# Optimization experiments

Measured on AMD Instinct MI355X. Metric: run time of the kernel, lower is better.

The kernel has to match this reference:

```python
import jax, jax.numpy as jnp
import numpy as np

B, N, XD = 4, 8192, 256   # batch, seq len, input/kv feature dim
F, H = 512, 8             # features, heads
D = F // H                # per-head dim = 64
EPS = 1e-6                # flax LayerNorm default epsilon


def _layer_norm(t, scale, bias):
    mu = jnp.mean(t, axis=-1, keepdims=True)
    var = jnp.mean(jnp.square(t - mu), axis=-1, keepdims=True)
    return (t - mu) * jax.lax.rsqrt(var + EPS) * scale + bias


def setup_inputs() -> dict:
    key = jax.random.key(0)
    ks = jax.random.split(key, 5)
    return {
        "x": jax.random.normal(ks[0], (B, N, XD), jnp.float32),
        "kv": jax.random.normal(ks[1], (B, N, XD), jnp.float32),
        # linen.initializers.normal(1/x_dim) / normal(1/h_dim)
        "Q": jax.random.normal(ks[2], (XD, F), jnp.float32) * (1.0 / XD),
        "K": jax.random.normal(ks[3], (XD, F), jnp.float32) * (1.0 / XD),
        "V": jax.random.normal(ks[4], (XD, F), jnp.float32) * (1.0 / XD),
        "log_scale": jnp.zeros((F,), jnp.float32),
        "ln_q_scale": jnp.ones((D,), jnp.float32),
        "ln_q_bias": jnp.zeros((D,), jnp.float32),
        "ln_k_scale": jnp.ones((D,), jnp.float32),
        "ln_k_bias": jnp.zeros((D,), jnp.float32),
        "ln_v_scale": jnp.ones((D,), jnp.float32),
        "ln_v_bias": jnp.zeros((D,), jnp.float32),
    }


def reference(x, kv, Q, K, V, log_scale,
              ln_q_scale, ln_q_bias, ln_k_scale, ln_k_bias, ln_v_scale, ln_v_bias):
    # QKV projections (value scaled by exp(log_scale) per feature)
    query = x @ Q                                    # [B, N, F]
    key = kv @ K                                     # [B, N, F]
    value = jnp.exp(log_scale) * (kv @ V)            # [B, N, F]
    # reshape exactly as the source module does
    q = query.reshape(B, H, -1, D)                   # [B, H, N, D]
    k = key.reshape(B, H, -1, D)
    v = value.reshape(B, H, -1, D)
    # per-head LayerNorm over the head dim (layer_norm=True)
    q = _layer_norm(q, ln_q_scale, ln_q_bias)
    k = _layer_norm(k, ln_k_scale, ln_k_bias)
    v = _layer_norm(v, ln_v_scale, ln_v_bias)
    # galerkin linear attention: Q @ (K^T V) / seq_len, no softmax, no NxN scores
    seq_len = k.shape[-2]
    ctx = jnp.einsum('bhnd,bhne->bhde', k, v)        # [B, H, D, D]
    out = jnp.einsum('bhnd,bhde->bhne', q, ctx) / seq_len
    return out.reshape(B, N, F)
```

## Files before the change

### kernel.cpp

```cpp
#include <hip/hip_runtime.h>
#include <stdint.h>

using f32x4  = __attribute__((ext_vector_type(4))) float;
using short8 = __attribute__((ext_vector_type(8))) short;

#define MFMA(a, b, c) __builtin_amdgcn_mfma_f32_16x16x32_bf16((a), (b), (c), 0, 0, 0)

#define GLOBAL_AS __attribute__((address_space(1)))
#define LDS_AS    __attribute__((address_space(3)))

#define XDIM 256
#define FDIM 512
#define EPS  1e-6f

#define QT_OFF    0u
#define KT_OFF    262144u
#define VT_OFF    524288u
#define CTXT_OFF  786432u
#define PART_OFF  1048576u

static __device__ __forceinline__ unsigned short f2bf(float f) {
  unsigned u = __float_as_uint(f);
  unsigned r = u + 0x7FFFu + ((u >> 16) & 1u);
  return (unsigned short)(r >> 16);
}

static __device__ __forceinline__ void async_copy16(const void* g, void* l) {
  __builtin_amdgcn_global_load_lds((GLOBAL_AS const void*)g, (LDS_AS void*)l, 16, 0, 0);
}

static __device__ __forceinline__ void stage_wpanel(const unsigned short* wt_panel, int ks,
                                                    int w, int lane, char* Blds) {
  const int cs = ((lane & 7) ^ ((lane >> 3) & 7)) << 4;
  const char* gbase = (const char*)wt_panel + (size_t)ks * 128 + cs;
#pragma unroll
  for (int i = 0; i < 8; ++i) {
    const int frow = w * 64 + i * 8 + (lane >> 3);
    async_copy16(gbase + (size_t)frow * 512, Blds + (size_t)(w * 64 + i * 8) * 128);
  }
}

static __device__ __forceinline__ void stage_a(const float* a_rows, int ks, int tid, char* Alds) {
  const int r = tid >> 2, cq = tid & 3;
  const float* s = a_rows + (size_t)r * XDIM + ks * 64 + cq * 16;
  float4 f0 = *(const float4*)(s);
  float4 f1 = *(const float4*)(s + 4);
  float4 f2 = *(const float4*)(s + 8);
  float4 f3 = *(const float4*)(s + 12);
  short8 v0, v1;
  v0[0] = (short)f2bf(f0.x); v0[1] = (short)f2bf(f0.y);
  v0[2] = (short)f2bf(f0.z); v0[3] = (short)f2bf(f0.w);
  v0[4] = (short)f2bf(f1.x); v0[5] = (short)f2bf(f1.y);
  v0[6] = (short)f2bf(f1.z); v0[7] = (short)f2bf(f1.w);
  v1[0] = (short)f2bf(f2.x); v1[1] = (short)f2bf(f2.y);
  v1[2] = (short)f2bf(f2.z); v1[3] = (short)f2bf(f2.w);
  v1[4] = (short)f2bf(f3.x); v1[5] = (short)f2bf(f3.y);
  v1[6] = (short)f2bf(f3.z); v1[7] = (short)f2bf(f3.w);
  *(short8*)(Alds + r * 144 + cq * 32)      = v0;
  *(short8*)(Alds + r * 144 + cq * 32 + 16) = v1;
}

static __device__ __forceinline__ void gemm_step(f32x4 acc[4][4], const char* Alds,
                                                 const char* Blds, int w, int lane) {
  const int lr = lane & 15, lk = lane >> 4;
#pragma unroll
  for (int s = 0; s < 2; ++s) {
    short8 a[4], b[4];
#pragma unroll
    for (int mt = 0; mt < 4; ++mt)
      a[mt] = *(const short8*)(Alds + (mt * 16 + lr) * 144 + s * 64 + lk * 16);
#pragma unroll
    for (int nt = 0; nt < 4; ++nt) {
      const int nf = w * 64 + nt * 16 + lr;
      b[nt] = *(const short8*)(Blds + (size_t)nf * 128 + ((s * 64 + lk * 16) ^ ((nf & 7) << 4)));
    }
#pragma unroll
    for (int mt = 0; mt < 4; ++mt)
#pragma unroll
      for (int nt = 0; nt < 4; ++nt)
        acc[mt][nt] = MFMA(a[mt], b[nt], acc[mt][nt]);
  }
}

static __device__ __forceinline__ void chunk_layernorm(f32x4 acc[4][4], const float* sc,
                                                       const float* bs, int lane) {
  const int lr = lane & 15;
  float scl[4], bia[4];
#pragma unroll
  for (int nt = 0; nt < 4; ++nt) { scl[nt] = sc[nt * 16 + lr]; bia[nt] = bs[nt * 16 + lr]; }
#pragma unroll
  for (int mt = 0; mt < 4; ++mt) {
#pragma unroll
    for (int j = 0; j < 4; ++j) {
      float a0 = acc[mt][0][j], a1 = acc[mt][1][j], a2 = acc[mt][2][j], a3 = acc[mt][3][j];
      float s  = a0 + a1 + a2 + a3;
      float s2 = a0 * a0 + a1 * a1 + a2 * a2 + a3 * a3;
#pragma unroll
      for (int off = 1; off < 16; off <<= 1) {
        s  += __shfl_xor(s, off, 16);
        s2 += __shfl_xor(s2, off, 16);
      }
      const float mu  = s * (1.0f / 64.0f);
      const float var = s2 * (1.0f / 64.0f) - mu * mu;
      const float rs  = rsqrtf(var + EPS);
#pragma unroll
      for (int nt = 0; nt < 4; ++nt)
        acc[mt][nt][j] = (acc[mt][nt][j] - mu) * rs * scl[nt] + bia[nt];
    }
  }
}

__global__ void prep_weights_kernel(const float* __restrict__ Q, const float* __restrict__ K,
                                    const float* __restrict__ V, const float* __restrict__ ls,
                                    unsigned short* __restrict__ Qt, unsigned short* __restrict__ Kt,
                                    unsigned short* __restrict__ Vt) {
  const int flat = blockIdx.x * 256 + threadIdx.x;
  const int mat = flat >> 17;
  const int rem = flat & 131071;
  const int f = rem & 511;
  const int k = rem >> 9;
  if (mat == 0)      Qt[f * 256 + k] = f2bf(Q[k * 512 + f]);
  else if (mat == 1) Kt[f * 256 + k] = f2bf(K[k * 512 + f]);
  else               Vt[f * 256 + k] = f2bf(V[k * 512 + f] * expf(ls[f]));
}

__launch_bounds__(256, 2)
__global__ void kv_ctx_kernel(const float* __restrict__ kv,
                              const unsigned short* __restrict__ Kt,
                              const unsigned short* __restrict__ Vt,
                              const float* __restrict__ lnk_s, const float* __restrict__ lnk_b,
                              const float* __restrict__ lnv_s, const float* __restrict__ lnv_b,
                              float* __restrict__ partials) {
  __shared__ __align__(16) char smem[41984];
  char* Alds = smem;
  char* Blds = smem + 9216;
  char* knT  = smem;
  char* vnT  = smem + 16384;

  const int tid = threadIdx.x, lane = tid & 63, w = tid >> 6;
  const int bid = blockIdx.x, rb = bid >> 1, nb = bid & 1;
  const int row0 = rb * 64;
  const int lr = lane & 15, lk = lane >> 4;

  const f32x4 z4 = {0.f, 0.f, 0.f, 0.f};
  f32x4 acck[4][4], accv[4][4];
#pragma unroll
  for (int i = 0; i < 4; ++i)
#pragma unroll
    for (int j = 0; j < 4; ++j) { acck[i][j] = z4; accv[i][j] = z4; }

  const float* arows = kv + (size_t)row0 * XDIM;
  const unsigned short* ktp = Kt + (size_t)(nb * 256) * 256;
  const unsigned short* vtp = Vt + (size_t)(nb * 256) * 256;

  for (int ks = 0; ks < 4; ++ks) {
    stage_a(arows, ks, tid, Alds);
    stage_wpanel(ktp, ks, w, lane, Blds);
    __syncthreads();
    gemm_step(acck, Alds, Blds, w, lane);
    __syncthreads();
    stage_wpanel(vtp, ks, w, lane, Blds);
    __syncthreads();
    gemm_step(accv, Alds, Blds, w, lane);
    __syncthreads();
  }

  chunk_layernorm(acck, lnk_s, lnk_b, lane);
  chunk_layernorm(accv, lnv_s, lnv_b, lane);

  f32x4 cacc[4];
#pragma unroll
  for (int i = 0; i < 4; ++i) cacc[i] = z4;

#pragma unroll
  for (int half = 0; half < 2; ++half) {
    if ((w >> 1) == half) {
      const int tbase = (w & 1) * 64;
#pragma unroll
      for (int mt = 0; mt < 4; ++mt)
#pragma unroll
        for (int j = 0; j < 4; ++j) {
          const int tt = tbase + mt * 16 + lk * 4 + j;
#pragma unroll
          for (int nt = 0; nt < 4; ++nt) {
            const int d = nt * 16 + lr;
            const int boff = d * 256 + ((tt * 2) ^ ((d & 7) << 4));
            *(unsigned short*)(knT + boff) = f2bf(acck[mt][nt][j]);
            *(unsigned short*)(vnT + boff) = f2bf(accv[mt][nt][j]);
          }
        }
    }
    __syncthreads();
    const int drow = w * 16 + lr;
#pragma unroll
    for (int s = 0; s < 4; ++s) {
      const short8 a = *(const short8*)(knT + drow * 256 + ((s * 64 + lk * 16) ^ ((drow & 7) << 4)));
#pragma unroll
      for (int nt = 0; nt < 4; ++nt) {
        const int e = nt * 16 + lr;
        const short8 b = *(const short8*)(vnT + e * 256 + ((s * 64 + lk * 16) ^ ((e & 7) << 4)));
        cacc[nt] = MFMA(a, b, cacc[nt]);
      }
    }
    __syncthreads();
  }

  float* pout = partials + (size_t)bid * 4096;
#pragma unroll
  for (int nt = 0; nt < 4; ++nt)
#pragma unroll
    for (int j = 0; j < 4; ++j) {
      const int d = w * 16 + lk * 4 + j;
      const int e = nt * 16 + lr;
      pout[d * 64 + e] = cacc[nt][j];
    }
}

__global__ void reduce_ctx_kernel(const float* __restrict__ partials,
                                  unsigned short* __restrict__ ctxTg) {
  const int bid = blockIdx.x, t = threadIdx.x;
  const int gg = bid >> 3, sl = bid & 7;
  const float* base = partials + (size_t)gg * 32 * 4096;
#pragma unroll
  for (int rep = 0; rep < 2; ++rep) {
    const int idx = sl * 512 + rep * 256 + t;
    float acc = 0.f;
#pragma unroll 8
    for (int p = 0; p < 32; ++p) acc += base[(size_t)p * 4096 + idx];
    const int d = idx >> 6, e = idx & 63;
    ctxTg[(size_t)gg * 4096 + e * 64 + d] = f2bf(acc * (1.0f / 8192.0f));
  }
}

__launch_bounds__(256, 2)
__global__ void q_out_kernel(const float* __restrict__ x, const unsigned short* __restrict__ Qt,
                             const unsigned short* __restrict__ ctxTg,
                             const float* __restrict__ lnq_s, const float* __restrict__ lnq_b,
                             float* __restrict__ out) {
  __shared__ __align__(16) char smem[41984];
  char* Alds = smem;
  char* Blds = smem + 9216;
  char* ctxT = smem;
  char* A2   = smem + 9216;

  const int tid = threadIdx.x, lane = tid & 63, w = tid >> 6;
  const int bid = blockIdx.x, rb = bid >> 1, nb = bid & 1;
  const int row0 = rb * 64;
  const int g = row0 >> 10;
  const int lr = lane & 15, lk = lane >> 4;

  const f32x4 z4 = {0.f, 0.f, 0.f, 0.f};
  f32x4 acc[4][4];
#pragma unroll
  for (int i = 0; i < 4; ++i)
#pragma unroll
    for (int j = 0; j < 4; ++j) acc[i][j] = z4;

  const float* arows = x + (size_t)row0 * XDIM;
  const unsigned short* qtp = Qt + (size_t)(nb * 256) * 256;

  for (int ks = 0; ks < 4; ++ks) {
    stage_a(arows, ks, tid, Alds);
    stage_wpanel(qtp, ks, w, lane, Blds);
    __syncthreads();
    gemm_step(acc, Alds, Blds, w, lane);
    __syncthreads();
  }

  chunk_layernorm(acc, lnq_s, lnq_b, lane);

  {
    const unsigned short* src = ctxTg + (size_t)g * 4096 + (tid >> 2) * 64 + (tid & 3) * 16;
    short8 c0 = *(const short8*)(src);
    short8 c1 = *(const short8*)(src + 8);
    char* dst = ctxT + (tid >> 2) * 144 + (tid & 3) * 32;
    *(short8*)dst        = c0;
    *(short8*)(dst + 16) = c1;
  }

#pragma unroll
  for (int mt = 0; mt < 4; ++mt)
#pragma unroll
    for (int j = 0; j < 4; ++j) {
      const int m = w * 64 + mt * 16 + lk * 4 + j;
#pragma unroll
      for (int nt = 0; nt < 4; ++nt) {
        const int d = nt * 16 + lr;
        *(unsigned short*)(A2 + (size_t)m * 128 + ((d * 2) ^ ((m & 7) << 4))) = f2bf(acc[mt][nt][j]);
      }
    }
  __syncthreads();

  f32x4 o[4][4];
#pragma unroll
  for (int i = 0; i < 4; ++i)
#pragma unroll
    for (int j = 0; j < 4; ++j) o[i][j] = z4;

#pragma unroll
  for (int s = 0; s < 2; ++s) {
    short8 a[4], b[4];
#pragma unroll
    for (int mt = 0; mt < 4; ++mt) {
      const int m = w * 64 + mt * 16 + lr;
      a[mt] = *(const short8*)(A2 + (size_t)m * 128 + ((s * 64 + lk * 16) ^ ((m & 7) << 4)));
    }
#pragma unroll
    for (int nt = 0; nt < 4; ++nt) {
      const int e = nt * 16 + lr;
      b[nt] = *(const short8*)(ctxT + e * 144 + s * 64 + lk * 16);
    }
#pragma unroll
    for (int mt = 0; mt < 4; ++mt)
#pragma unroll
      for (int nt = 0; nt < 4; ++nt)
        o[mt][nt] = MFMA(a[mt], b[nt], o[mt][nt]);
  }

#pragma unroll
  for (int mt = 0; mt < 4; ++mt)
#pragma unroll
    for (int nt = 0; nt < 4; ++nt)
#pragma unroll
      for (int j = 0; j < 4; ++j) {
        const int m = w * 64 + mt * 16 + lk * 4 + j;
        const int col = nb * 256 + (m >> 6) * 64 + nt * 16 + lr;
        out[(size_t)(row0 + (m & 63)) * FDIM + col] = o[mt][nt][j];
      }
}

extern "C" void kernel_launch(void* const* d_in, const int* in_sizes, int n_in,
                              void* d_out, int out_size, void* d_ws, size_t ws_size,
                              hipStream_t stream) {
  (void)in_sizes; (void)n_in; (void)out_size; (void)ws_size;
  const float* x     = (const float*)d_in[0];
  const float* kv    = (const float*)d_in[1];
  const float* Q     = (const float*)d_in[2];
  const float* K     = (const float*)d_in[3];
  const float* V     = (const float*)d_in[4];
  const float* ls    = (const float*)d_in[5];
  const float* lnq_s = (const float*)d_in[6];
  const float* lnq_b = (const float*)d_in[7];
  const float* lnk_s = (const float*)d_in[8];
  const float* lnk_b = (const float*)d_in[9];
  const float* lnv_s = (const float*)d_in[10];
  const float* lnv_b = (const float*)d_in[11];
  float* out = (float*)d_out;

  char* ws = (char*)d_ws;
  unsigned short* Qt   = (unsigned short*)(ws + QT_OFF);
  unsigned short* Kt   = (unsigned short*)(ws + KT_OFF);
  unsigned short* Vt   = (unsigned short*)(ws + VT_OFF);
  unsigned short* ctxT = (unsigned short*)(ws + CTXT_OFF);
  float* partials      = (float*)(ws + PART_OFF);

  prep_weights_kernel<<<1536, 256, 0, stream>>>(Q, K, V, ls, Qt, Kt, Vt);
  kv_ctx_kernel<<<1024, 256, 0, stream>>>(kv, Kt, Vt, lnk_s, lnk_b, lnv_s, lnv_b, partials);
  reduce_ctx_kernel<<<256, 256, 0, stream>>>(partials, ctxT);
  q_out_kernel<<<1024, 256, 0, stream>>>(x, Qt, ctxT, lnq_s, lnq_b, out);
}
```

Baseline: 106.5 us.

## Stage full A tile once and read weight fragments directly from global

Both projection kernels now convert the whole 64x256 activation tile to bf16 in LDS once, with one barrier, instead of staging a slice per k-step. The weight panels are no longer copied into LDS asynchronously; each wave loads its B fragments straight from global memory (L2-resident bf16 weights), which removes the per-k-step barriers. The LDS reuse for the context and output phases is reorganised with packed 4-wide bf16 stores and fewer barriers. The trade-off is global-load latency on the MFMA critical path with no software prefetch, in exchange for less synchronisation.

Result: slower. 125.9 us (+18.1%).

```diff
diff --git a/kernel.cpp b/kernel.cpp
--- a/kernel.cpp
+++ b/kernel.cpp
@@ -3,11 +3,9 @@
 
 using f32x4  = __attribute__((ext_vector_type(4))) float;
 using short8 = __attribute__((ext_vector_type(8))) short;
+using u16x4  = __attribute__((ext_vector_type(4))) unsigned short;
 
 #define MFMA(a, b, c) __builtin_amdgcn_mfma_f32_16x16x32_bf16((a), (b), (c), 0, 0, 0)
-
-#define GLOBAL_AS __attribute__((address_space(1)))
-#define LDS_AS    __attribute__((address_space(3)))
 
 #define XDIM 256
 #define FDIM 512
@@ -25,60 +23,27 @@
   return (unsigned short)(r >> 16);
 }
 
-static __device__ __forceinline__ void async_copy16(const void* g, void* l) {
-  __builtin_amdgcn_global_load_lds((GLOBAL_AS const void*)g, (LDS_AS void*)l, 16, 0, 0);
-}
-
-static __device__ __forceinline__ void stage_wpanel(const unsigned short* wt_panel, int ks,
-                                                    int w, int lane, char* Blds) {
-  const int cs = ((lane & 7) ^ ((lane >> 3) & 7)) << 4;
-  const char* gbase = (const char*)wt_panel + (size_t)ks * 128 + cs;
-#pragma unroll
-  for (int i = 0; i < 8; ++i) {
-    const int frow = w * 64 + i * 8 + (lane >> 3);
-    async_copy16(gbase + (size_t)frow * 512, Blds + (size_t)(w * 64 + i * 8) * 128);
-  }
-}
-
-static __device__ __forceinline__ void stage_a(const float* a_rows, int ks, int tid, char* Alds) {
+static __device__ __forceinline__ void stage_a_full(const float* a_rows, int tid, char* Alds) {
   const int r = tid >> 2, cq = tid & 3;
-  const float* s = a_rows + (size_t)r * XDIM + ks * 64 + cq * 16;
-  float4 f0 = *(const float4*)(s);
-  float4 f1 = *(const float4*)(s + 4);
-  float4 f2 = *(const float4*)(s + 8);
-  float4 f3 = *(const float4*)(s + 12);
-  short8 v0, v1;
-  v0[0] = (short)f2bf(f0.x); v0[1] = (short)f2bf(f0.y);
-  v0[2] = (short)f2bf(f0.z); v0[3] = (short)f2bf(f0.w);
-  v0[4] = (short)f2bf(f1.x); v0[5] = (short)f2bf(f1.y);
-  v0[6] = (short)f2bf(f1.z); v0[7] = (short)f2bf(f1.w);
-  v1[0] = (short)f2bf(f2.x); v1[1] = (short)f2bf(f2.y);
-  v1[2] = (short)f2bf(f2.z); v1[3] = (short)f2bf(f2.w);
-  v1[4] = (short)f2bf(f3.x); v1[5] = (short)f2bf(f3.y);
-  v1[6] = (short)f2bf(f3.z); v1[7] = (short)f2bf(f3.w);
-  *(short8*)(Alds + r * 144 + cq * 32)      = v0;
-  *(short8*)(Alds + r * 144 + cq * 32 + 16) = v1;
-}
-
-static __device__ __forceinline__ void gemm_step(f32x4 acc[4][4], const char* Alds,
-                                                 const char* Blds, int w, int lane) {
-  const int lr = lane & 15, lk = lane >> 4;
-#pragma unroll
-  for (int s = 0; s < 2; ++s) {
-    short8 a[4], b[4];
-#pragma unroll
-    for (int mt = 0; mt < 4; ++mt)
-      a[mt] = *(const short8*)(Alds + (mt * 16 + lr) * 144 + s * 64 + lk * 16);
-#pragma unroll
-    for (int nt = 0; nt < 4; ++nt) {
-      const int nf = w * 64 + nt * 16 + lr;
-      b[nt] = *(const short8*)(Blds + (size_t)nf * 128 + ((s * 64 + lk * 16) ^ ((nf & 7) << 4)));
-    }
-#pragma unroll
-    for (int mt = 0; mt < 4; ++mt)
-#pragma unroll
-      for (int nt = 0; nt < 4; ++nt)
-        acc[mt][nt] = MFMA(a[mt], b[nt], acc[mt][nt]);
+  const float* src = a_rows + (size_t)r * XDIM + cq * 64;
+  char* dst = Alds + r * 528 + cq * 128;
+#pragma unroll
+  for (int i = 0; i < 4; ++i) {
+    float4 f0 = *(const float4*)(src + i * 16);
+    float4 f1 = *(const float4*)(src + i * 16 + 4);
+    float4 f2 = *(const float4*)(src + i * 16 + 8);
+    float4 f3 = *(const float4*)(src + i * 16 + 12);
+    short8 v0, v1;
+    v0[0] = (short)f2bf(f0.x); v0[1] = (short)f2bf(f0.y);
+    v0[2] = (short)f2bf(f0.z); v0[3] = (short)f2bf(f0.w);
+    v0[4] = (short)f2bf(f1.x); v0[5] = (short)f2bf(f1.y);
+    v0[6] = (short)f2bf(f1.z); v0[7] = (short)f2bf(f1.w);
+    v1[0] = (short)f2bf(f2.x); v1[1] = (short)f2bf(f2.y);
+    v1[2] = (short)f2bf(f2.z); v1[3] = (short)f2bf(f2.w);
+    v1[4] = (short)f2bf(f3.x); v1[5] = (short)f2bf(f3.y);
+    v1[6] = (short)f2bf(f3.z); v1[7] = (short)f2bf(f3.w);
+    *(short8*)(dst + i * 32)      = v0;
+    *(short8*)(dst + i * 32 + 16) = v1;
   }
 }
 
@@ -131,16 +96,15 @@
                               const float* __restrict__ lnk_s, const float* __restrict__ lnk_b,
                               const float* __restrict__ lnv_s, const float* __restrict__ lnv_b,
                               float* __restrict__ partials) {
-  __shared__ __align__(16) char smem[41984];
-  char* Alds = smem;
-  char* Blds = smem + 9216;
-  char* knT  = smem;
-  char* vnT  = smem + 16384;
+  __shared__ __align__(16) char smem[33792];
 
   const int tid = threadIdx.x, lane = tid & 63, w = tid >> 6;
   const int bid = blockIdx.x, rb = bid >> 1, nb = bid & 1;
   const int row0 = rb * 64;
   const int lr = lane & 15, lk = lane >> 4;
+  const int koff = lk * 16;
+
+  stage_a_full(kv + (size_t)row0 * XDIM, tid, smem);
 
   const f32x4 z4 = {0.f, 0.f, 0.f, 0.f};
   f32x4 acck[4][4], accv[4][4];
@@ -149,71 +113,106 @@
 #pragma unroll
     for (int j = 0; j < 4; ++j) { acck[i][j] = z4; accv[i][j] = z4; }
 
-  const float* arows = kv + (size_t)row0 * XDIM;
-  const unsigned short* ktp = Kt + (size_t)(nb * 256) * 256;
-  const unsigned short* vtp = Vt + (size_t)(nb * 256) * 256;
-
+  const char* kbase = (const char*)Kt + (size_t)(nb * 256 + w * 64) * 512;
+  const char* vbase = (const char*)Vt + (size_t)(nb * 256 + w * 64) * 512;
+
+  __syncthreads();
+
+#pragma unroll
   for (int ks = 0; ks < 4; ++ks) {
-    stage_a(arows, ks, tid, Alds);
-    stage_wpanel(ktp, ks, w, lane, Blds);
-    __syncthreads();
-    gemm_step(acck, Alds, Blds, w, lane);
-    __syncthreads();
-    stage_wpanel(vtp, ks, w, lane, Blds);
-    __syncthreads();
-    gemm_step(accv, Alds, Blds, w, lane);
-    __syncthreads();
+    short8 a0[4], a1[4];
+#pragma unroll
+    for (int mt = 0; mt < 4; ++mt) {
+      const char* ar = smem + (mt * 16 + lr) * 528 + ks * 128;
+      a0[mt] = *(const short8*)(ar + koff);
+      a1[mt] = *(const short8*)(ar + 64 + koff);
+    }
+    {
+      short8 b0[4], b1[4];
+#pragma unroll
+      for (int nt = 0; nt < 4; ++nt) {
+        const char* kr = kbase + (size_t)(nt * 16 + lr) * 512 + ks * 128 + koff;
+        b0[nt] = *(const short8*)(kr);
+        b1[nt] = *(const short8*)(kr + 64);
+      }
+#pragma unroll
+      for (int mt = 0; mt < 4; ++mt)
+#pragma unroll
+        for (int nt = 0; nt < 4; ++nt) {
+          acck[mt][nt] = MFMA(a0[mt], b0[nt], acck[mt][nt]);
+          acck[mt][nt] = MFMA(a1[mt], b1[nt], acck[mt][nt]);
+        }
+    }
+    {
+      short8 b0[4], b1[4];
+#pragma unroll
+      for (int nt = 0; nt < 4; ++nt) {
+        const char* vr = vbase + (size_t)(nt * 16 + lr) * 512 + ks * 128 + koff;
+        b0[nt] = *(const short8*)(vr);
+        b1[nt] = *(const short8*)(vr + 64);
+      }
+#pragma unroll
+      for (int mt = 0; mt < 4; ++mt)
+#pragma unroll
+        for (int nt = 0; nt < 4; ++nt) {
+          accv[mt][nt] = MFMA(a0[mt], b0[nt], accv[mt][nt]);
+          accv[mt][nt] = MFMA(a1[mt], b1[nt], accv[mt][nt]);
+        }
+    }
   }
 
   chunk_layernorm(acck, lnk_s, lnk_b, lane);
   chunk_layernorm(accv, lnv_s, lnv_b, lane);
 
+  char* knT = smem;
+  char* vnT = smem + 16384;
   f32x4 cacc[4];
 #pragma unroll
   for (int i = 0; i < 4; ++i) cacc[i] = z4;
+  const int drow = w * 16 + lr;
 
 #pragma unroll
   for (int half = 0; half < 2; ++half) {
+    __syncthreads();
     if ((w >> 1) == half) {
-      const int tbase = (w & 1) * 64;
-#pragma unroll
-      for (int mt = 0; mt < 4; ++mt)
-#pragma unroll
-        for (int j = 0; j < 4; ++j) {
-          const int tt = tbase + mt * 16 + lk * 4 + j;
-#pragma unroll
-          for (int nt = 0; nt < 4; ++nt) {
-            const int d = nt * 16 + lr;
-            const int boff = d * 256 + ((tt * 2) ^ ((d & 7) << 4));
-            *(unsigned short*)(knT + boff) = f2bf(acck[mt][nt][j]);
-            *(unsigned short*)(vnT + boff) = f2bf(accv[mt][nt][j]);
+      const int tb2 = (w & 1) * 128;
+#pragma unroll
+      for (int mt = 0; mt < 4; ++mt) {
+        const int tb = tb2 + mt * 32 + lk * 8;
+#pragma unroll
+        for (int nt = 0; nt < 4; ++nt) {
+          const int d = nt * 16 + lr;
+          u16x4 pk, pv;
+#pragma unroll
+          for (int j = 0; j < 4; ++j) {
+            pk[j] = f2bf(acck[mt][nt][j]);
+            pv[j] = f2bf(accv[mt][nt][j]);
           }
+          const int boff = d * 256 + (tb ^ ((d & 7) << 4));
+          *(u16x4*)(knT + boff) = pk;
+          *(u16x4*)(vnT + boff) = pv;
         }
+      }
     }
     __syncthreads();
-    const int drow = w * 16 + lr;
 #pragma unroll
     for (int s = 0; s < 4; ++s) {
-      const short8 a = *(const short8*)(knT + drow * 256 + ((s * 64 + lk * 16) ^ ((drow & 7) << 4)));
+      const short8 a = *(const short8*)(knT + drow * 256 + ((s * 64 + koff) ^ ((drow & 7) << 4)));
 #pragma unroll
       for (int nt = 0; nt < 4; ++nt) {
         const int e = nt * 16 + lr;
-        const short8 b = *(const short8*)(vnT + e * 256 + ((s * 64 + lk * 16) ^ ((e & 7) << 4)));
+        const short8 b = *(const short8*)(vnT + e * 256 + ((s * 64 + koff) ^ ((e & 7) << 4)));
         cacc[nt] = MFMA(a, b, cacc[nt]);
       }
     }
-    __syncthreads();
   }
 
   float* pout = partials + (size_t)bid * 4096;
 #pragma unroll
   for (int nt = 0; nt < 4; ++nt)
 #pragma unroll
-    for (int j = 0; j < 4; ++j) {
-      const int d = w * 16 + lk * 4 + j;
-      const int e = nt * 16 + lr;
-      pout[d * 64 + e] = cacc[nt][j];
-    }
+    for (int j = 0; j < 4; ++j)
+      pout[(w * 16 + lk * 4 + j) * 64 + nt * 16 + lr] = cacc[nt][j];
 }
 
 __global__ void reduce_ctx_kernel(const float* __restrict__ partials,
@@ -237,17 +236,24 @@
                              const unsigned short* __restrict__ ctxTg,
                              const float* __restrict__ lnq_s, const float* __restrict__ lnq_b,
                              float* __restrict__ out) {
-  __shared__ __align__(16) char smem[41984];
-  char* Alds = smem;
-  char* Blds = smem + 9216;
-  char* ctxT = smem;
-  char* A2   = smem + 9216;
+  __shared__ __align__(16) char smem[43008];
 
   const int tid = threadIdx.x, lane = tid & 63, w = tid >> 6;
   const int bid = blockIdx.x, rb = bid >> 1, nb = bid & 1;
   const int row0 = rb * 64;
   const int g = row0 >> 10;
   const int lr = lane & 15, lk = lane >> 4;
+  const int koff = lk * 16;
+  char* ctxT = smem + 33792;
+
+  stage_a_full(x + (size_t)row0 * XDIM, tid, smem);
+
+  {
+    const unsigned short* src = ctxTg + (size_t)g * 4096 + (tid >> 2) * 64 + (tid & 3) * 16;
+    char* dst = ctxT + (tid >> 2) * 144 + (tid & 3) * 32;
+    *(short8*)dst        = *(const short8*)(src);
+    *(short8*)(dst + 16) = *(const short8*)(src + 8);
+  }
 
   const f32x4 z4 = {0.f, 0.f, 0.f, 0.f};
   f32x4 acc[4][4];
@@ -256,37 +262,49 @@
 #pragma unroll
     for (int j = 0; j < 4; ++j) acc[i][j] = z4;
 
-  const float* arows = x + (size_t)row0 * XDIM;
-  const unsigned short* qtp = Qt + (size_t)(nb * 256) * 256;
-
+  const char* qbase = (const char*)Qt + (size_t)(nb * 256 + w * 64) * 512;
+
+  __syncthreads();
+
+#pragma unroll
   for (int ks = 0; ks < 4; ++ks) {
-    stage_a(arows, ks, tid, Alds);
-    stage_wpanel(qtp, ks, w, lane, Blds);
-    __syncthreads();
-    gemm_step(acc, Alds, Blds, w, lane);
-    __syncthreads();
+    short8 a0[4], a1[4], b0[4], b1[4];
+#pragma unroll
+    for (int mt = 0; mt < 4; ++mt) {
+      const char* ar = smem + (mt * 16 + lr) * 528 + ks * 128;
+      a0[mt] = *(const short8*)(ar + koff);
+      a1[mt] = *(const short8*)(ar + 64 + koff);
+    }
+#pragma unroll
+    for (int nt = 0; nt < 4; ++nt) {
+      const char* qr = qbase + (size_t)(nt * 16 + lr) * 512 + ks * 128 + koff;
+      b0[nt] = *(const short8*)(qr);
+      b1[nt] = *(const short8*)(qr + 64);
+    }
+#pragma unroll
+    for (int mt = 0; mt < 4; ++mt)
+#pragma unroll
+      for (int nt = 0; nt < 4; ++nt) {
+        acc[mt][nt] = MFMA(a0[mt], b0[nt], acc[mt][nt]);
+        acc[mt][nt] = MFMA(a1[mt], b1[nt], acc[mt][nt]);
+      }
   }
 
   chunk_layernorm(acc, lnq_s, lnq_b, lane);
 
-  {
-    const unsigned short* src = ctxTg + (size_t)g * 4096 + (tid >> 2) * 64 + (tid & 3) * 16;
-    short8 c0 = *(const short8*)(src);
-    short8 c1 = *(const short8*)(src + 8);
-    char* dst = ctxT + (tid >> 2) * 144 + (tid & 3) * 32;
-    *(short8*)dst        = c0;
-    *(short8*)(dst + 16) = c1;
-  }
-
+  __syncthreads();
+
+  char* A2 = smem + w * 8192;
 #pragma unroll
   for (int mt = 0; mt < 4; ++mt)
 #pragma unroll
     for (int j = 0; j < 4; ++j) {
-      const int m = w * 64 + mt * 16 + lk * 4 + j;
+      const int m = mt * 16 + lk * 4 + j;
+      const int sw = (m & 7) << 4;
 #pragma unroll
       for (int nt = 0; nt < 4; ++nt) {
         const int d = nt * 16 + lr;
-        *(unsigned short*)(A2 + (size_t)m * 128 + ((d * 2) ^ ((m & 7) << 4))) = f2bf(acc[mt][nt][j]);
+        *(unsigned short*)(A2 + m * 128 + ((d * 2) ^ sw)) = f2bf(acc[mt][nt][j]);
       }
     }
   __syncthreads();
@@ -302,14 +320,12 @@
     short8 a[4], b[4];
 #pragma unroll
     for (int mt = 0; mt < 4; ++mt) {
-      const int m = w * 64 + mt * 16 + lr;
-      a[mt] = *(const short8*)(A2 + (size_t)m * 128 + ((s * 64 + lk * 16) ^ ((m & 7) << 4)));
-    }
-#pragma unroll
-    for (int nt = 0; nt < 4; ++nt) {
-      const int e = nt * 16 + lr;
-      b[nt] = *(const short8*)(ctxT + e * 144 + s * 64 + lk * 16);
-    }
+      const int m = mt * 16 + lr;
+      a[mt] = *(const short8*)(A2 + m * 128 + ((s * 64 + koff) ^ ((m & 7) << 4)));
+    }
+#pragma unroll
+    for (int nt = 0; nt < 4; ++nt)
+      b[nt] = *(const short8*)(ctxT + (nt * 16 + lr) * 144 + s * 64 + koff);
 #pragma unroll
     for (int mt = 0; mt < 4; ++mt)
 #pragma unroll
@@ -323,9 +339,8 @@
     for (int nt = 0; nt < 4; ++nt)
 #pragma unroll
       for (int j = 0; j < 4; ++j) {
-        const int m = w * 64 + mt * 16 + lk * 4 + j;
-        const int col = nb * 256 + (m >> 6) * 64 + nt * 16 + lr;
-        out[(size_t)(row0 + (m & 63)) * FDIM + col] = o[mt][nt][j];
+        const int n = mt * 16 + lk * 4 + j;
+        out[(size_t)(row0 + n) * FDIM + nb * 256 + w * 64 + nt * 16 + lr] = o[mt][nt][j];
       }
 }
 
```
